# Kernel tuning notes

Measured on AMD Instinct MI355X. Metric: run time of the kernel, lower is better.

The kernel has to match this reference:

```python
import jax, jax.numpy as jnp
import numpy as np

CLIP = 7.0          # cfg.swiglu_clip
AUX_COEF = 0.02     # cfg.router_aux_loss_coef
TOP_K = 4           # cfg.experts_per_token


def setup_inputs() -> dict:
    key = jax.random.key(0)
    ks = jax.random.split(key, 4)
    H, E, FF = 1024, 16, 1024
    B, T = 2, 1024
    std = 0.02
    return {
        "x": jax.random.normal(ks[0], (B, T, H), jnp.float32),
        "W_in": jax.random.normal(ks[1], (E, H, 2 * FF), jnp.float32) * std,
        "b_in": jnp.zeros((E, 2 * FF), jnp.float32),
        "W_out": jax.random.normal(ks[2], (E, FF, H), jnp.float32) * std,
        "b_out": jnp.zeros((E, H), jnp.float32),
        "router_w": jax.random.normal(ks[3], (E, H), jnp.float32) * std,
        "router_b": jnp.zeros((E,), jnp.float32),
    }


def reference(x, W_in, b_in, W_out, b_out, router_w, router_b):
    B, T, H = x.shape
    E = W_in.shape[0]
    S = B * T
    x_flat = x.reshape(S, H)

    # --- router + top-k gating ---
    logits = x_flat @ router_w.T + router_b                         # [S, E]
    topk_w, topk_i = jax.lax.top_k(logits, TOP_K)                   # [S, K]
    topk_w = jax.nn.softmax(topk_w.astype(jnp.float32), axis=-1).astype(x.dtype)

    # --- aux load-balance loss (faithful to source, incl. argmax-over-indices) ---
    probs = jax.nn.softmax(logits.astype(jnp.float32), axis=-1)     # [S, E]
    importance = probs.mean(axis=0)                                 # [E]
    load = jax.nn.one_hot(jnp.argmax(topk_i, axis=-1), E, dtype=jnp.float32).mean(axis=0)
    aux_loss = AUX_COEF * E * jnp.sum(importance * load)

    # scatter top-k weights to dense [S, E] combine weights
    final_w = jnp.zeros((S, E), x.dtype).at[jnp.arange(S)[:, None], topk_i].add(topk_w)

    # --- dense per-expert SwiGLU FFN (every expert for every token) ---
    h = jnp.einsum('sh,ehd->sed', x_flat, W_in) + b_in              # [S, E, 2*FF]
    up, gate = jnp.split(h, 2, axis=-1)                             # chunk(2, -1)
    up = jnp.clip(up, -CLIP, CLIP)
    gate = jnp.clip(gate, -CLIP, CLIP)
    act = jax.nn.silu(gate) * up                                    # [S, E, FF]
    eo = jnp.einsum('sef,efh->seh', act, W_out) + b_out             # [S, E, H]

    out = jnp.einsum('seh,se->sh', eo, final_w).reshape(B, T, H)
    return out, aux_loss
```

## Files before the change

kernel.cpp:

```cpp
#include <hip/hip_runtime.h>
#include <math.h>

#define S_TOK 2048
#define H_DIM 1024
#define E_NUM 16
#define FF_DIM 1024
#define TOPK 4
#define CLIPV 7.0f
#define AUXC 0.02f
#define BK 32
#define NT (H_DIM / BK)

typedef short bf16x8 __attribute__((ext_vector_type(8)));
typedef float f32x4 __attribute__((ext_vector_type(4)));

__device__ __forceinline__ unsigned short f2bf(float f) {
  unsigned int u = __float_as_uint(f);
  u += 0x7fffu + ((u >> 16) & 1u);
  return (unsigned short)(u >> 16);
}

__device__ __forceinline__ void gload16(const void* g, void* l) {
  __builtin_amdgcn_global_load_lds((const __attribute__((address_space(1))) void*)g,
                                   (__attribute__((address_space(3))) void*)l, 16, 0, 0);
}

__device__ __forceinline__ int imin(int a, int b) { return a < b ? a : b; }

__global__ void logits_kernel(const float* __restrict__ x, const float* __restrict__ rw,
                              const float* __restrict__ rb, float* __restrict__ logits,
                              unsigned short* __restrict__ xb) {
  int tok = blockIdx.x * 4 + (threadIdx.x >> 6);
  int lane = threadIdx.x & 63;
  const float4* xr = (const float4*)(x + (size_t)tok * H_DIM);
  ushort4* xbw = (ushort4*)(xb + (size_t)tok * H_DIM);
  float p[E_NUM];
#pragma unroll
  for (int e = 0; e < E_NUM; ++e) p[e] = 0.f;
#pragma unroll
  for (int it = 0; it < 4; ++it) {
    float4 xv = xr[it * 64 + lane];
    ushort4 o;
    o.x = f2bf(xv.x); o.y = f2bf(xv.y); o.z = f2bf(xv.z); o.w = f2bf(xv.w);
    xbw[it * 64 + lane] = o;
#pragma unroll
    for (int e = 0; e < E_NUM; ++e) {
      float4 wv = ((const float4*)(rw + (size_t)e * H_DIM))[it * 64 + lane];
      p[e] += xv.x * wv.x + xv.y * wv.y + xv.z * wv.z + xv.w * wv.w;
    }
  }
#pragma unroll
  for (int e = 0; e < E_NUM; ++e) {
#pragma unroll
    for (int off = 32; off > 0; off >>= 1) p[e] += __shfl_xor(p[e], off);
  }
  if (lane == 0) {
    float4* lp = (float4*)&logits[tok * E_NUM];
#pragma unroll
    for (int q = 0; q < 4; ++q)
      lp[q] = make_float4(p[q * 4 + 0] + rb[q * 4 + 0], p[q * 4 + 1] + rb[q * 4 + 1],
                          p[q * 4 + 2] + rb[q * 4 + 2], p[q * 4 + 3] + rb[q * 4 + 3]);
  }
}

__global__ __launch_bounds__(256) void topk_kernel(const float* __restrict__ logits,
                                                   int* __restrict__ topk_i, float* __restrict__ topk_w,
                                                   int* __restrict__ counts, float* __restrict__ imp,
                                                   int* __restrict__ pos_cnt) {
  __shared__ float s_imp[E_NUM];
  __shared__ int s_cnt[E_NUM];
  __shared__ int s_pos[TOPK];
  int tid = threadIdx.x;
  if (tid < E_NUM) { s_imp[tid] = 0.f; s_cnt[tid] = 0; }
  if (tid < TOPK) s_pos[tid] = 0;
  __syncthreads();

  int t = blockIdx.x * 256 + tid;
  float lg[E_NUM];
  {
    const float4* lp = (const float4*)&logits[t * E_NUM];
#pragma unroll
    for (int q = 0; q < 4; ++q) {
      float4 v = lp[q];
      lg[q * 4 + 0] = v.x; lg[q * 4 + 1] = v.y; lg[q * 4 + 2] = v.z; lg[q * 4 + 3] = v.w;
    }
  }
  int idx[TOPK]; float val[TOPK];
  float tmp[E_NUM];
#pragma unroll
  for (int e = 0; e < E_NUM; ++e) tmp[e] = lg[e];
#pragma unroll
  for (int k = 0; k < TOPK; ++k) {
    float best = -INFINITY; int bi = 0;
#pragma unroll
    for (int e = 0; e < E_NUM; ++e) if (tmp[e] > best) { best = tmp[e]; bi = e; }
    val[k] = best; idx[k] = bi; tmp[bi] = -INFINITY;
  }
  float ssum = 0.f, wv[TOPK];
#pragma unroll
  for (int k = 0; k < TOPK; ++k) { wv[k] = expf(val[k] - val[0]); ssum += wv[k]; }
#pragma unroll
  for (int k = 0; k < TOPK; ++k) wv[k] /= ssum;
#pragma unroll
  for (int k = 0; k < TOPK; ++k) {
    topk_i[t * TOPK + k] = idx[k];
    topk_w[t * TOPK + k] = wv[k];
  }
  float se = 0.f, pr[E_NUM];
#pragma unroll
  for (int e = 0; e < E_NUM; ++e) { pr[e] = expf(lg[e] - val[0]); se += pr[e]; }
  float inv = 1.f / se;
  int mi = idx[0], pos = 0;
#pragma unroll
  for (int k = 1; k < TOPK; ++k) if (idx[k] > mi) { mi = idx[k]; pos = k; }

  int lane = tid & 63;
#pragma unroll
  for (int e = 0; e < E_NUM; ++e) {
    float v = pr[e] * inv;
    int c = (idx[0] == e) + (idx[1] == e) + (idx[2] == e) + (idx[3] == e);
#pragma unroll
    for (int off = 32; off > 0; off >>= 1) {
      v += __shfl_xor(v, off);
      c += __shfl_xor(c, off);
    }
    if (lane == 0) {
      atomicAdd(&s_imp[e], v);
      atomicAdd(&s_cnt[e], c);
    }
  }
#pragma unroll
  for (int k = 0; k < TOPK; ++k) {
    int pc = (pos == k) ? 1 : 0;
#pragma unroll
    for (int off = 32; off > 0; off >>= 1) pc += __shfl_xor(pc, off);
    if (lane == 0) atomicAdd(&s_pos[k], pc);
  }
  __syncthreads();
  if (tid < E_NUM) {
    atomicAdd(&imp[tid], s_imp[tid]);
    atomicAdd(&counts[tid], s_cnt[tid]);
  }
  if (tid < TOPK) atomicAdd(&pos_cnt[tid], s_pos[tid]);
}

__global__ void scan_kernel(const int* __restrict__ counts, int* __restrict__ offsets) {
  if (threadIdx.x == 0) {
    int off = 0;
    for (int e = 0; e < E_NUM; ++e) { offsets[e] = off; off += counts[e]; }
    offsets[E_NUM] = off;
  }
}

__global__ __launch_bounds__(256) void assign_kernel(
    const int* __restrict__ topk_i, const int* __restrict__ offsets, int* __restrict__ cursor,
    int* __restrict__ tok_list, int* __restrict__ slot_of) {
  __shared__ int s_cnt[E_NUM];
  __shared__ int s_base[E_NUM];
  int tid = threadIdx.x;
  if (tid < E_NUM) s_cnt[tid] = 0;
  __syncthreads();
  int t = blockIdx.x * 256 + tid;
  int e[TOPK], lslot[TOPK];
#pragma unroll
  for (int k = 0; k < TOPK; ++k) {
    e[k] = topk_i[t * TOPK + k];
    lslot[k] = atomicAdd(&s_cnt[e[k]], 1);
  }
  __syncthreads();
  if (tid < E_NUM) s_base[tid] = atomicAdd(&cursor[tid], s_cnt[tid]);
  __syncthreads();
#pragma unroll
  for (int k = 0; k < TOPK; ++k) {
    int slot = offsets[e[k]] + s_base[e[k]] + lslot[k];
    tok_list[slot] = t;
    slot_of[t * TOPK + k] = slot;
  }
}

__global__ void transpose_kernel(const float* __restrict__ in, unsigned short* __restrict__ out,
                                 int R, int C) {
  __shared__ float tile[64][65];
  int e = blockIdx.z;
  in  += (size_t)e * R * C;
  out += (size_t)e * R * C;
  int r0 = blockIdx.y * 64, c0 = blockIdx.x * 64;
  int tx = threadIdx.x & 15, ty = threadIdx.x >> 4;
#pragma unroll
  for (int j = 0; j < 4; ++j) {
    int r = ty + j * 16;
    float4 v = *(const float4*)&in[(size_t)(r0 + r) * C + c0 + tx * 4];
    tile[r][tx * 4 + 0] = v.x; tile[r][tx * 4 + 1] = v.y;
    tile[r][tx * 4 + 2] = v.z; tile[r][tx * 4 + 3] = v.w;
  }
  __syncthreads();
#pragma unroll
  for (int j = 0; j < 4; ++j) {
    int c = ty + j * 16;
    ushort4 o;
    o.x = f2bf(tile[tx * 4 + 0][c]);
    o.y = f2bf(tile[tx * 4 + 1][c]);
    o.z = f2bf(tile[tx * 4 + 2][c]);
    o.w = f2bf(tile[tx * 4 + 3][c]);
    *(ushort4*)&out[(size_t)(c0 + c) * R + r0 + tx * 4] = o;
  }
}

__global__ __launch_bounds__(256, 2) void gemm1_kernel(
    const unsigned short* __restrict__ xb, const unsigned short* __restrict__ winT,
    const float* __restrict__ b_in, const int* __restrict__ offsets,
    const int* __restrict__ tok_list, unsigned short* __restrict__ act) {
  __shared__ unsigned short ldsA[2][128 * BK];
  __shared__ unsigned short ldsB[2][256 * BK];
  const int lin = blockIdx.x;
  const int nid = (lin & 7) * 256 + (lin >> 3);
  const int e  = nid >> 7;
  const int mt = (nid & 127) >> 3;
  const int nt = nid & 7;
  const int base = offsets[e];
  const int cnt = offsets[e + 1] - base;
  if (mt * 128 >= cnt) return;
  const int n0f = nt * 128;
  const int tid = threadIdx.x, w = tid >> 6, lane = tid & 63;

  const int arow = w * 16 + (lane >> 2);
  const int t0 = tok_list[base + imin(mt * 128 + arow, cnt - 1)];
  const int t1 = tok_list[base + imin(mt * 128 + arow + 64, cnt - 1)];
  const unsigned short* gA0 = xb + (size_t)t0 * H_DIM + (lane & 3) * 8;
  const unsigned short* gA1 = xb + (size_t)t1 * H_DIM + (lane & 3) * 8;
  auto brow_f = [&](int r) {
    int f = n0f + ((r >> 5) << 4) + (r & 15);
    return ((r >> 4) & 1) ? (FF_DIM + f) : f;
  };
  const unsigned short* we = winT + (size_t)e * 2 * FF_DIM * H_DIM;
  const unsigned short* gB0 = we + (size_t)brow_f(arow)       * H_DIM + (lane & 3) * 8;
  const unsigned short* gB1 = we + (size_t)brow_f(arow + 64)  * H_DIM + (lane & 3) * 8;
  const unsigned short* gB2 = we + (size_t)brow_f(arow + 128) * H_DIM + (lane & 3) * 8;
  const unsigned short* gB3 = we + (size_t)brow_f(arow + 192) * H_DIM + (lane & 3) * 8;

  f32x4 acc[8][4];
#pragma unroll
  for (int m = 0; m < 8; ++m)
#pragma unroll
    for (int n = 0; n < 4; ++n) acc[m][n] = (f32x4){0.f, 0.f, 0.f, 0.f};

#define STAGE1(buf, k0)                                     \
  do {                                                      \
    gload16(gA0 + (k0), &ldsA[buf][w * 512]);               \
    gload16(gA1 + (k0), &ldsA[buf][w * 512 + 2048]);        \
    gload16(gB0 + (k0), &ldsB[buf][w * 512]);               \
    gload16(gB1 + (k0), &ldsB[buf][w * 512 + 2048]);        \
    gload16(gB2 + (k0), &ldsB[buf][w * 512 + 4096]);        \
    gload16(gB3 + (k0), &ldsB[buf][w * 512 + 6144]);        \
  } while (0)

  STAGE1(0, 0);
  __syncthreads();
  int buf = 0;
  const int ko = (lane >> 4) * 8;
  for (int kt = 0; kt < NT; ++kt) {
    if (kt + 1 < NT) STAGE1(buf ^ 1, (kt + 1) * BK);
    bf16x8 a[8], b[4];
#pragma unroll
    for (int mf = 0; mf < 8; ++mf)
      a[mf] = *(const bf16x8*)&ldsA[buf][(mf * 16 + (lane & 15)) * BK + ko];
#pragma unroll
    for (int nf = 0; nf < 4; ++nf)
      b[nf] = *(const bf16x8*)&ldsB[buf][(w * 64 + nf * 16 + (lane & 15)) * BK + ko];
#pragma unroll
    for (int mf = 0; mf < 8; ++mf)
#pragma unroll
      for (int nf = 0; nf < 4; ++nf)
        acc[mf][nf] = __builtin_amdgcn_mfma_f32_16x16x32_bf16(a[mf], b[nf], acc[mf][nf], 0, 0, 0);
    __syncthreads();
    buf ^= 1;
  }

  const float* bin = b_in + (size_t)e * 2 * FF_DIM;
#pragma unroll
  for (int mf = 0; mf < 8; ++mf) {
    int rbase = mf * 16 + (lane >> 4) * 4;
#pragma unroll
    for (int p = 0; p < 2; ++p) {
      int f = n0f + (w * 2 + p) * 16 + (lane & 15);
      float bu = bin[f], bg = bin[FF_DIM + f];
#pragma unroll
      for (int i = 0; i < 4; ++i) {
        int mrow = mt * 128 + rbase + i;
        if (mrow < cnt) {
          float up = acc[mf][2 * p][i] + bu;
          float gt = acc[mf][2 * p + 1][i] + bg;
          up = fminf(fmaxf(up, -CLIPV), CLIPV);
          gt = fminf(fmaxf(gt, -CLIPV), CLIPV);
          float av = (gt / (1.f + expf(-gt))) * up;
          act[(size_t)(base + mrow) * FF_DIM + f] = f2bf(av);
        }
      }
    }
  }
}

__global__ __launch_bounds__(256, 2) void gemm2_kernel(
    const unsigned short* __restrict__ act, const unsigned short* __restrict__ woutT,
    const float* __restrict__ b_out, const int* __restrict__ offsets,
    float* __restrict__ eo) {
  __shared__ unsigned short ldsA[2][128 * BK];
  __shared__ unsigned short ldsB[2][256 * BK];
  const int lin = blockIdx.x;
  const int nid = (lin & 7) * 128 + (lin >> 3);
  const int e = nid >> 6;
  const int rem = nid & 63;
  const int mt = rem >> 2;
  const int nt = rem & 3;
  const int base = offsets[e];
  const int cnt = offsets[e + 1] - base;
  if (mt * 128 >= cnt) return;
  const int n0 = nt * 256;
  const int tid = threadIdx.x, w = tid >> 6, lane = tid & 63;

  const int arow = w * 16 + (lane >> 2);
  const int m0_ = imin(mt * 128 + arow, cnt - 1);
  const int m1_ = imin(mt * 128 + arow + 64, cnt - 1);
  const int kbase = (lane & 3) * 8;
  const unsigned short* gA0 = act + (size_t)(base + m0_) * FF_DIM + kbase;
  const unsigned short* gA1 = act + (size_t)(base + m1_) * FF_DIM + kbase;
  const unsigned short* we = woutT + (size_t)e * H_DIM * FF_DIM;
  const unsigned short* gB0 = we + (size_t)(n0 + arow)       * FF_DIM + kbase;
  const unsigned short* gB1 = we + (size_t)(n0 + arow + 64)  * FF_DIM + kbase;
  const unsigned short* gB2 = we + (size_t)(n0 + arow + 128) * FF_DIM + kbase;
  const unsigned short* gB3 = we + (size_t)(n0 + arow + 192) * FF_DIM + kbase;

  f32x4 acc[8][4];
#pragma unroll
  for (int m = 0; m < 8; ++m)
#pragma unroll
    for (int n = 0; n < 4; ++n) acc[m][n] = (f32x4){0.f, 0.f, 0.f, 0.f};

#define STAGE2(buf, k0)                                     \
  do {                                                      \
    gload16(gA0 + (k0), &ldsA[buf][w * 512]);               \
    gload16(gA1 + (k0), &ldsA[buf][w * 512 + 2048]);        \
    gload16(gB0 + (k0), &ldsB[buf][w * 512]);               \
    gload16(gB1 + (k0), &ldsB[buf][w * 512 + 2048]);        \
    gload16(gB2 + (k0), &ldsB[buf][w * 512 + 4096]);        \
    gload16(gB3 + (k0), &ldsB[buf][w * 512 + 6144]);        \
  } while (0)

  STAGE2(0, 0);
  __syncthreads();
  int buf = 0;
  const int ko = (lane >> 4) * 8;
  for (int kt = 0; kt < FF_DIM / BK; ++kt) {
    if (kt + 1 < FF_DIM / BK) STAGE2(buf ^ 1, (kt + 1) * BK);
    bf16x8 a[8], b[4];
#pragma unroll
    for (int mf = 0; mf < 8; ++mf)
      a[mf] = *(const bf16x8*)&ldsA[buf][(mf * 16 + (lane & 15)) * BK + ko];
#pragma unroll
    for (int nf = 0; nf < 4; ++nf)
      b[nf] = *(const bf16x8*)&ldsB[buf][(w * 64 + nf * 16 + (lane & 15)) * BK + ko];
#pragma unroll
    for (int mf = 0; mf < 8; ++mf)
#pragma unroll
      for (int nf = 0; nf < 4; ++nf)
        acc[mf][nf] = __builtin_amdgcn_mfma_f32_16x16x32_bf16(a[mf], b[nf], acc[mf][nf], 0, 0, 0);
    __syncthreads();
    buf ^= 1;
  }

  const float* bo = b_out + (size_t)e * H_DIM;
#pragma unroll
  for (int mf = 0; mf < 8; ++mf) {
#pragma unroll
    for (int i = 0; i < 4; ++i) {
      int mrow = mt * 128 + mf * 16 + (lane >> 4) * 4 + i;
      if (mrow < cnt) {
        float* row = eo + (size_t)(base + mrow) * H_DIM;
#pragma unroll
        for (int nf = 0; nf < 4; ++nf) {
          int h = n0 + w * 64 + nf * 16 + (lane & 15);
          row[h] = acc[mf][nf][i] + bo[h];
        }
      }
    }
  }
}

__global__ __launch_bounds__(256) void combine_kernel(
    const float* __restrict__ eo, const float* __restrict__ topk_w,
    const int* __restrict__ slot_of, float* __restrict__ out) {
  int t = blockIdx.x;
  int tid = threadIdx.x;
  float4 r = make_float4(0.f, 0.f, 0.f, 0.f);
#pragma unroll
  for (int k = 0; k < TOPK; ++k) {
    int s = slot_of[t * TOPK + k];
    float wv = topk_w[t * TOPK + k];
    float4 v = ((const float4*)(eo + (size_t)s * H_DIM))[tid];
    r.x = fmaf(wv, v.x, r.x);
    r.y = fmaf(wv, v.y, r.y);
    r.z = fmaf(wv, v.z, r.z);
    r.w = fmaf(wv, v.w, r.w);
  }
  ((float4*)(out + (size_t)t * H_DIM))[tid] = r;
}

__global__ void finalize_kernel(const float* __restrict__ imp, const int* __restrict__ pos_cnt,
                                float* __restrict__ out_aux) {
  if (threadIdx.x == 0) {
    float s = 0.f;
    for (int p = 0; p < TOPK; ++p)
      s += (imp[p] / (float)S_TOK) * ((float)pos_cnt[p] / (float)S_TOK);
    *out_aux = AUXC * (float)E_NUM * s;
  }
}

extern "C" void kernel_launch(void* const* d_in, const int* in_sizes, int n_in,
                              void* d_out, int out_size, void* d_ws, size_t ws_size,
                              hipStream_t stream) {
  const float* x     = (const float*)d_in[0];
  const float* W_in  = (const float*)d_in[1];
  const float* b_in  = (const float*)d_in[2];
  const float* W_out = (const float*)d_in[3];
  const float* b_out = (const float*)d_in[4];
  const float* rw    = (const float*)d_in[5];
  const float* rb    = (const float*)d_in[6];
  float* out = (float*)d_out;

  char* ws = (char*)d_ws;
  size_t off = 0;
  auto alloc = [&](size_t bytes) {
    void* p = ws + off;
    off = (off + bytes + 255) & ~(size_t)255;
    return p;
  };
  unsigned short* xb    = (unsigned short*)alloc((size_t)S_TOK * H_DIM * 2);
  unsigned short* winT  = (unsigned short*)alloc((size_t)E_NUM * 2 * FF_DIM * H_DIM * 2);
  unsigned short* woutT = (unsigned short*)alloc((size_t)E_NUM * H_DIM * FF_DIM * 2);
  unsigned short* act   = (unsigned short*)alloc((size_t)S_TOK * TOPK * FF_DIM * 2);
  float* eo      = (float*)alloc((size_t)S_TOK * TOPK * H_DIM * 4);
  float* logits  = (float*)alloc((size_t)S_TOK * E_NUM * 4);
  int*   topk_i  = (int*)alloc(S_TOK * TOPK * 4);
  float* topk_w  = (float*)alloc(S_TOK * TOPK * 4);
  int*   tok_list= (int*)alloc(S_TOK * TOPK * 4);
  int*   slot_of = (int*)alloc(S_TOK * TOPK * 4);
  int* ctrl = (int*)alloc(64 * 4);
  int* counts = ctrl;
  int* cursor = ctrl + 16;
  int* pos_cnt = ctrl + 32;
  float* imp = (float*)(ctrl + 48);
  int* offsets = (int*)alloc(32 * 4);

  hipMemsetAsync(ctrl, 0, 64 * 4, stream);

  logits_kernel<<<S_TOK / 4, 256, 0, stream>>>(x, rw, rb, logits, xb);
  transpose_kernel<<<dim3(2 * FF_DIM / 64, H_DIM / 64, E_NUM), 256, 0, stream>>>(W_in, winT, H_DIM, 2 * FF_DIM);
  transpose_kernel<<<dim3(H_DIM / 64, FF_DIM / 64, E_NUM), 256, 0, stream>>>(W_out, woutT, FF_DIM, H_DIM);
  topk_kernel<<<S_TOK / 256, 256, 0, stream>>>(logits, topk_i, topk_w, counts, imp, pos_cnt);
  scan_kernel<<<1, 64, 0, stream>>>(counts, offsets);
  assign_kernel<<<S_TOK / 256, 256, 0, stream>>>(topk_i, offsets, cursor, tok_list, slot_of);
  gemm1_kernel<<<2048, 256, 0, stream>>>(xb, winT, b_in, offsets, tok_list, act);
  gemm2_kernel<<<1024, 256, 0, stream>>>(act, woutT, b_out, offsets, eo);
  combine_kernel<<<S_TOK, 256, 0, stream>>>(eo, topk_w, slot_of, out);
  finalize_kernel<<<1, 64, 0, stream>>>(imp, pos_cnt, out + (size_t)S_TOK * H_DIM);
}
```

Measured before the change: 224.3 us.

## Triple-buffer LDS pipeline with explicit vmcnt waits and remap tile order

Both grouped GEMM kernels move from double- to triple-buffered LDS staging. They prefetch two K-tiles ahead and use explicit s_waitcnt vmcnt counts plus raw s_barrier in place of __syncthreads, so global loads overlap more with MFMA work. The block-to-tile mapping also changes so that mt is the fastest-varying index, which groups blocks that share weight columns for L2 reuse. The extra LDS buffer (72KB per block) may cut occupancy below the two blocks per CU requested by the launch bounds. The hand-written vmcnt counts are fragile if the compiler reorders or splits the loads.

```diff
diff --git a/kernel.cpp b/kernel.cpp
--- a/kernel.cpp
+++ b/kernel.cpp
@@ -210,13 +210,13 @@
     const unsigned short* __restrict__ xb, const unsigned short* __restrict__ winT,
     const float* __restrict__ b_in, const int* __restrict__ offsets,
     const int* __restrict__ tok_list, unsigned short* __restrict__ act) {
-  __shared__ unsigned short ldsA[2][128 * BK];
-  __shared__ unsigned short ldsB[2][256 * BK];
+  __shared__ unsigned short ldsA[3][128 * BK];
+  __shared__ unsigned short ldsB[3][256 * BK];
   const int lin = blockIdx.x;
   const int nid = (lin & 7) * 256 + (lin >> 3);
   const int e  = nid >> 7;
-  const int mt = (nid & 127) >> 3;
-  const int nt = nid & 7;
+  const int nt = (nid >> 4) & 7;
+  const int mt = nid & 15;
   const int base = offsets[e];
   const int cnt = offsets[e + 1] - base;
   if (mt * 128 >= cnt) return;
@@ -255,12 +255,21 @@
   } while (0)
 
   STAGE1(0, 0);
-  __syncthreads();
+  STAGE1(1, BK);
   int buf = 0;
-  const int ko = (lane >> 4) * 8;
   for (int kt = 0; kt < NT; ++kt) {
-    if (kt + 1 < NT) STAGE1(buf ^ 1, (kt + 1) * BK);
+    int nb = buf + 2; if (nb >= 3) nb -= 3;
+    if (kt + 2 < NT) {
+      STAGE1(nb, (kt + 2) * BK);
+      asm volatile("s_waitcnt vmcnt(12)" ::: "memory");
+    } else if (kt + 2 == NT) {
+      asm volatile("s_waitcnt vmcnt(6)" ::: "memory");
+    } else {
+      asm volatile("s_waitcnt vmcnt(0)" ::: "memory");
+    }
+    __builtin_amdgcn_s_barrier();
     bf16x8 a[8], b[4];
+    const int ko = (lane >> 4) * 8;
 #pragma unroll
     for (int mf = 0; mf < 8; ++mf)
       a[mf] = *(const bf16x8*)&ldsA[buf][(mf * 16 + (lane & 15)) * BK + ko];
@@ -272,8 +281,8 @@
 #pragma unroll
       for (int nf = 0; nf < 4; ++nf)
         acc[mf][nf] = __builtin_amdgcn_mfma_f32_16x16x32_bf16(a[mf], b[nf], acc[mf][nf], 0, 0, 0);
-    __syncthreads();
-    buf ^= 1;
+    __builtin_amdgcn_s_barrier();
+    buf = (buf == 2) ? 0 : buf + 1;
   }
 
   const float* bin = b_in + (size_t)e * 2 * FF_DIM;
@@ -304,14 +313,13 @@
     const unsigned short* __restrict__ act, const unsigned short* __restrict__ woutT,
     const float* __restrict__ b_out, const int* __restrict__ offsets,
     float* __restrict__ eo) {
-  __shared__ unsigned short ldsA[2][128 * BK];
-  __shared__ unsigned short ldsB[2][256 * BK];
+  __shared__ unsigned short ldsA[3][128 * BK];
+  __shared__ unsigned short ldsB[3][256 * BK];
   const int lin = blockIdx.x;
   const int nid = (lin & 7) * 128 + (lin >> 3);
   const int e = nid >> 6;
-  const int rem = nid & 63;
-  const int mt = rem >> 2;
-  const int nt = rem & 3;
+  const int nt = (nid >> 4) & 3;
+  const int mt = nid & 15;
   const int base = offsets[e];
   const int cnt = offsets[e + 1] - base;
   if (mt * 128 >= cnt) return;
@@ -347,12 +355,21 @@
   } while (0)
 
   STAGE2(0, 0);
-  __syncthreads();
+  STAGE2(1, BK);
   int buf = 0;
-  const int ko = (lane >> 4) * 8;
   for (int kt = 0; kt < FF_DIM / BK; ++kt) {
-    if (kt + 1 < FF_DIM / BK) STAGE2(buf ^ 1, (kt + 1) * BK);
+    int nb = buf + 2; if (nb >= 3) nb -= 3;
+    if (kt + 2 < FF_DIM / BK) {
+      STAGE2(nb, (kt + 2) * BK);
+      asm volatile("s_waitcnt vmcnt(12)" ::: "memory");
+    } else if (kt + 2 == FF_DIM / BK) {
+      asm volatile("s_waitcnt vmcnt(6)" ::: "memory");
+    } else {
+      asm volatile("s_waitcnt vmcnt(0)" ::: "memory");
+    }
+    __builtin_amdgcn_s_barrier();
     bf16x8 a[8], b[4];
+    const int ko = (lane >> 4) * 8;
 #pragma unroll
     for (int mf = 0; mf < 8; ++mf)
       a[mf] = *(const bf16x8*)&ldsA[buf][(mf * 16 + (lane & 15)) * BK + ko];
@@ -364,8 +381,8 @@
 #pragma unroll
       for (int nf = 0; nf < 4; ++nf)
         acc[mf][nf] = __builtin_amdgcn_mfma_f32_16x16x32_bf16(a[mf], b[nf], acc[mf][nf], 0, 0, 0);
-    __syncthreads();
-    buf ^= 1;
+    __builtin_amdgcn_s_barrier();
+    buf = (buf == 2) ? 0 : buf + 1;
   }
 
   const float* bo = b_out + (size_t)e * H_DIM;
```

New measurement: 216.3 us. -3.6%, faster.

## Rework expert GEMMs into 8-wave 256x256 tiles with swizzled LDS pipeline

Applied to the files above, without the earlier changes.

Both grouped expert GEMMs now use 512-thread blocks computing 256x256 output tiles. The K loop is split into 32-wide half-steps across a double-buffered 128KB LDS ring, and direct global-to-LDS loads are interleaved phase by phase with MFMA bursts. Explicit barriers, vmcnt waits and s_setprio control the overlap, and an XOR swizzle on LDS chunks is meant to avoid bank conflicts. The aim is more operand reuse per load and better hiding of memory latency behind MFMA work. In exchange, occupancy drops to one block per CU, and the larger M tile can waste more work when an expert's token count is uneven.

```diff
diff --git a/kernel.cpp b/kernel.cpp
--- a/kernel.cpp
+++ b/kernel.cpp
@@ -8,8 +8,6 @@
 #define TOPK 4
 #define CLIPV 7.0f
 #define AUXC 0.02f
-#define BK 32
-#define NT (H_DIM / BK)
 
 typedef short bf16x8 __attribute__((ext_vector_type(8)));
 typedef float f32x4 __attribute__((ext_vector_type(4)));
@@ -206,90 +204,132 @@
   }
 }
 
-__global__ __launch_bounds__(256, 2) void gemm1_kernel(
+#define A_LDS(buf, ks)  (((buf) * 2 + (ks)) * 16384)
+#define B_LDS(buf, ks)  (65536 + ((buf) * 2 + (ks)) * 16384)
+
+#define PHASE(buf, mh, ks, STAGE, VMC)                                          \
+  do {                                                                          \
+    bf16x8 a_[4];                                                               \
+    _Pragma("unroll") for (int m_ = 0; m_ < 4; ++m_)                            \
+      a_[m_] = *(const bf16x8*)(ldsc + A_LDS(buf, ks) +                         \
+                                (lrow_a + ((mh)*4 + m_) * 16) * 64 + lchunk);   \
+    if ((mh) == 0) {                                                            \
+      _Pragma("unroll") for (int n_ = 0; n_ < 4; ++n_)                          \
+        bq[n_] = *(const bf16x8*)(ldsc + B_LDS(buf, ks) +                       \
+                                  (lrow_b + n_ * 16) * 64 + lchunk);            \
+    }                                                                           \
+    STAGE;                                                                      \
+    __builtin_amdgcn_s_barrier();                                               \
+    asm volatile("s_waitcnt lgkmcnt(0)" ::: "memory");                          \
+    __builtin_amdgcn_sched_barrier(0);                                          \
+    __builtin_amdgcn_s_setprio(1);                                              \
+    _Pragma("unroll") for (int m_ = 0; m_ < 4; ++m_)                            \
+      _Pragma("unroll") for (int n_ = 0; n_ < 4; ++n_)                          \
+        acc[(mh)*4 + m_][n_] = __builtin_amdgcn_mfma_f32_16x16x32_bf16(         \
+            a_[m_], bq[n_], acc[(mh)*4 + m_][n_], 0, 0, 0);                     \
+    __builtin_amdgcn_s_setprio(0);                                              \
+    asm volatile("s_waitcnt vmcnt(" #VMC ")" ::: "memory");                     \
+    __builtin_amdgcn_s_barrier();                                               \
+  } while (0)
+
+#define NOP do {} while (0)
+
+__global__ __launch_bounds__(512, 2) void gemm1_kernel(
     const unsigned short* __restrict__ xb, const unsigned short* __restrict__ winT,
     const float* __restrict__ b_in, const int* __restrict__ offsets,
     const int* __restrict__ tok_list, unsigned short* __restrict__ act) {
-  __shared__ unsigned short ldsA[2][128 * BK];
-  __shared__ unsigned short ldsB[2][256 * BK];
+  __shared__ __align__(16) unsigned short lds[65536];
   const int lin = blockIdx.x;
-  const int nid = (lin & 7) * 256 + (lin >> 3);
-  const int e  = nid >> 7;
-  const int mt = (nid & 127) >> 3;
-  const int nt = nid & 7;
+  const int nid = (lin & 7) * 128 + (lin >> 3);
+  const int e  = nid >> 6;
+  const int nt = (nid >> 3) & 7;
+  const int mt = nid & 7;
   const int base = offsets[e];
   const int cnt = offsets[e + 1] - base;
-  if (mt * 128 >= cnt) return;
+  if (mt * 256 >= cnt) return;
   const int n0f = nt * 128;
-  const int tid = threadIdx.x, w = tid >> 6, lane = tid & 63;
-
-  const int arow = w * 16 + (lane >> 2);
-  const int t0 = tok_list[base + imin(mt * 128 + arow, cnt - 1)];
-  const int t1 = tok_list[base + imin(mt * 128 + arow + 64, cnt - 1)];
-  const unsigned short* gA0 = xb + (size_t)t0 * H_DIM + (lane & 3) * 8;
-  const unsigned short* gA1 = xb + (size_t)t1 * H_DIM + (lane & 3) * 8;
+  const int tid = threadIdx.x, W = tid >> 6, l = tid & 63;
+  const int wr = W >> 2, wc = W & 3;
+
+  const int c_src = (l & 3) ^ ((l >> 3) & 3);
+  const int rd0 = (W * 2 + 0) * 16 + (l >> 2);
+  const int rd1 = (W * 2 + 1) * 16 + (l >> 2);
+  const int tA0 = tok_list[base + imin(mt * 256 + rd0, cnt - 1)];
+  const int tA1 = tok_list[base + imin(mt * 256 + rd1, cnt - 1)];
+  const unsigned short* pA0 = xb + (size_t)tA0 * H_DIM + c_src * 8;
+  const unsigned short* pA1 = xb + (size_t)tA1 * H_DIM + c_src * 8;
   auto brow_f = [&](int r) {
     int f = n0f + ((r >> 5) << 4) + (r & 15);
     return ((r >> 4) & 1) ? (FF_DIM + f) : f;
   };
   const unsigned short* we = winT + (size_t)e * 2 * FF_DIM * H_DIM;
-  const unsigned short* gB0 = we + (size_t)brow_f(arow)       * H_DIM + (lane & 3) * 8;
-  const unsigned short* gB1 = we + (size_t)brow_f(arow + 64)  * H_DIM + (lane & 3) * 8;
-  const unsigned short* gB2 = we + (size_t)brow_f(arow + 128) * H_DIM + (lane & 3) * 8;
-  const unsigned short* gB3 = we + (size_t)brow_f(arow + 192) * H_DIM + (lane & 3) * 8;
+  const unsigned short* pB0 = we + (size_t)brow_f(rd0) * H_DIM + c_src * 8;
+  const unsigned short* pB1 = we + (size_t)brow_f(rd1) * H_DIM + c_src * 8;
+  const int sseg = W * 2048;
+
+#define STA(kt, ks, buf)                                                        \
+  do {                                                                          \
+    gload16(pA0 + (kt) * 64 + (ks) * 32, (char*)lds + A_LDS(buf, ks) + sseg);   \
+    gload16(pA1 + (kt) * 64 + (ks) * 32, (char*)lds + A_LDS(buf, ks) + sseg + 1024); \
+  } while (0)
+#define STB(kt, ks, buf)                                                        \
+  do {                                                                          \
+    gload16(pB0 + (kt) * 64 + (ks) * 32, (char*)lds + B_LDS(buf, ks) + sseg);   \
+    gload16(pB1 + (kt) * 64 + (ks) * 32, (char*)lds + B_LDS(buf, ks) + sseg + 1024); \
+  } while (0)
+
+  const char* ldsc = (const char*)lds;
+  const int lrow_a = wr * 128 + (l & 15);
+  const int lrow_b = wc * 64 + (l & 15);
+  const int lchunk = ((l >> 4) * 16) ^ (((l >> 1) & 3) << 4);
 
   f32x4 acc[8][4];
 #pragma unroll
   for (int m = 0; m < 8; ++m)
 #pragma unroll
     for (int n = 0; n < 4; ++n) acc[m][n] = (f32x4){0.f, 0.f, 0.f, 0.f};
-
-#define STAGE1(buf, k0)                                     \
-  do {                                                      \
-    gload16(gA0 + (k0), &ldsA[buf][w * 512]);               \
-    gload16(gA1 + (k0), &ldsA[buf][w * 512 + 2048]);        \
-    gload16(gB0 + (k0), &ldsB[buf][w * 512]);               \
-    gload16(gB1 + (k0), &ldsB[buf][w * 512 + 2048]);        \
-    gload16(gB2 + (k0), &ldsB[buf][w * 512 + 4096]);        \
-    gload16(gB3 + (k0), &ldsB[buf][w * 512 + 6144]);        \
-  } while (0)
-
-  STAGE1(0, 0);
-  __syncthreads();
-  int buf = 0;
-  const int ko = (lane >> 4) * 8;
-  for (int kt = 0; kt < NT; ++kt) {
-    if (kt + 1 < NT) STAGE1(buf ^ 1, (kt + 1) * BK);
-    bf16x8 a[8], b[4];
-#pragma unroll
-    for (int mf = 0; mf < 8; ++mf)
-      a[mf] = *(const bf16x8*)&ldsA[buf][(mf * 16 + (lane & 15)) * BK + ko];
-#pragma unroll
-    for (int nf = 0; nf < 4; ++nf)
-      b[nf] = *(const bf16x8*)&ldsB[buf][(w * 64 + nf * 16 + (lane & 15)) * BK + ko];
-#pragma unroll
-    for (int mf = 0; mf < 8; ++mf)
-#pragma unroll
-      for (int nf = 0; nf < 4; ++nf)
-        acc[mf][nf] = __builtin_amdgcn_mfma_f32_16x16x32_bf16(a[mf], b[nf], acc[mf][nf], 0, 0, 0);
-    __syncthreads();
-    buf ^= 1;
-  }
+  bf16x8 bq[4];
+
+  STA(0, 0, 0); STB(0, 0, 0); STA(0, 1, 0); STB(0, 1, 0); STA(1, 0, 1); STB(1, 0, 1);
+  asm volatile("s_waitcnt vmcnt(8)" ::: "memory");
+  __builtin_amdgcn_s_barrier();
+
+  for (int i = 0; i < 7; ++i) {
+    const int k0 = 2 * i;
+    PHASE(0, 0, 0, STA(k0 + 1, 1, 1), 8);
+    PHASE(0, 1, 0, STB(k0 + 1, 1, 1), 8);
+    PHASE(0, 0, 1, STA(k0 + 2, 0, 0), 8);
+    PHASE(0, 1, 1, STB(k0 + 2, 0, 0), 8);
+    PHASE(1, 0, 0, STA(k0 + 2, 1, 0), 8);
+    PHASE(1, 1, 0, STB(k0 + 2, 1, 0), 8);
+    PHASE(1, 0, 1, STA(k0 + 3, 0, 1), 8);
+    PHASE(1, 1, 1, STB(k0 + 3, 0, 1), 8);
+  }
+  PHASE(0, 0, 0, STA(15, 1, 1), 8);
+  PHASE(0, 1, 0, STB(15, 1, 1), 8);
+  PHASE(0, 0, 1, NOP, 8);
+  PHASE(0, 1, 1, NOP, 4);
+  PHASE(1, 0, 0, NOP, 4);
+  PHASE(1, 1, 0, NOP, 0);
+  PHASE(1, 0, 1, NOP, 0);
+  PHASE(1, 1, 1, NOP, 0);
+#undef STA
+#undef STB
 
   const float* bin = b_in + (size_t)e * 2 * FF_DIM;
 #pragma unroll
-  for (int mf = 0; mf < 8; ++mf) {
-    int rbase = mf * 16 + (lane >> 4) * 4;
+  for (int m = 0; m < 8; ++m) {
+    int mrow0 = mt * 256 + wr * 128 + m * 16 + (l >> 4) * 4;
 #pragma unroll
     for (int p = 0; p < 2; ++p) {
-      int f = n0f + (w * 2 + p) * 16 + (lane & 15);
+      int f = n0f + (wc * 2 + p) * 16 + (l & 15);
       float bu = bin[f], bg = bin[FF_DIM + f];
 #pragma unroll
-      for (int i = 0; i < 4; ++i) {
-        int mrow = mt * 128 + rbase + i;
+      for (int i2 = 0; i2 < 4; ++i2) {
+        int mrow = mrow0 + i2;
         if (mrow < cnt) {
-          float up = acc[mf][2 * p][i] + bu;
-          float gt = acc[mf][2 * p + 1][i] + bg;
+          float up = acc[m][2 * p][i2] + bu;
+          float gt = acc[m][2 * p + 1][i2] + bg;
           up = fminf(fmaxf(up, -CLIPV), CLIPV);
           gt = fminf(fmaxf(gt, -CLIPV), CLIPV);
           float av = (gt / (1.f + expf(-gt))) * up;
@@ -300,86 +340,97 @@
   }
 }
 
-__global__ __launch_bounds__(256, 2) void gemm2_kernel(
+__global__ __launch_bounds__(512, 2) void gemm2_kernel(
     const unsigned short* __restrict__ act, const unsigned short* __restrict__ woutT,
     const float* __restrict__ b_out, const int* __restrict__ offsets,
     float* __restrict__ eo) {
-  __shared__ unsigned short ldsA[2][128 * BK];
-  __shared__ unsigned short ldsB[2][256 * BK];
+  __shared__ __align__(16) unsigned short lds[65536];
   const int lin = blockIdx.x;
-  const int nid = (lin & 7) * 128 + (lin >> 3);
-  const int e = nid >> 6;
-  const int rem = nid & 63;
-  const int mt = rem >> 2;
-  const int nt = rem & 3;
+  const int nid = (lin & 7) * 64 + (lin >> 3);
+  const int e  = nid >> 5;
+  const int nt = (nid >> 3) & 3;
+  const int mt = nid & 7;
   const int base = offsets[e];
   const int cnt = offsets[e + 1] - base;
-  if (mt * 128 >= cnt) return;
+  if (mt * 256 >= cnt) return;
   const int n0 = nt * 256;
-  const int tid = threadIdx.x, w = tid >> 6, lane = tid & 63;
-
-  const int arow = w * 16 + (lane >> 2);
-  const int m0_ = imin(mt * 128 + arow, cnt - 1);
-  const int m1_ = imin(mt * 128 + arow + 64, cnt - 1);
-  const int kbase = (lane & 3) * 8;
-  const unsigned short* gA0 = act + (size_t)(base + m0_) * FF_DIM + kbase;
-  const unsigned short* gA1 = act + (size_t)(base + m1_) * FF_DIM + kbase;
+  const int tid = threadIdx.x, W = tid >> 6, l = tid & 63;
+  const int wr = W >> 2, wc = W & 3;
+
+  const int c_src = (l & 3) ^ ((l >> 3) & 3);
+  const int rd0 = (W * 2 + 0) * 16 + (l >> 2);
+  const int rd1 = (W * 2 + 1) * 16 + (l >> 2);
+  const int r0_ = imin(mt * 256 + rd0, cnt - 1);
+  const int r1_ = imin(mt * 256 + rd1, cnt - 1);
+  const unsigned short* pA0 = act + (size_t)(base + r0_) * FF_DIM + c_src * 8;
+  const unsigned short* pA1 = act + (size_t)(base + r1_) * FF_DIM + c_src * 8;
   const unsigned short* we = woutT + (size_t)e * H_DIM * FF_DIM;
-  const unsigned short* gB0 = we + (size_t)(n0 + arow)       * FF_DIM + kbase;
-  const unsigned short* gB1 = we + (size_t)(n0 + arow + 64)  * FF_DIM + kbase;
-  const unsigned short* gB2 = we + (size_t)(n0 + arow + 128) * FF_DIM + kbase;
-  const unsigned short* gB3 = we + (size_t)(n0 + arow + 192) * FF_DIM + kbase;
+  const unsigned short* pB0 = we + (size_t)(n0 + rd0) * FF_DIM + c_src * 8;
+  const unsigned short* pB1 = we + (size_t)(n0 + rd1) * FF_DIM + c_src * 8;
+  const int sseg = W * 2048;
+
+#define STA(kt, ks, buf)                                                        \
+  do {                                                                          \
+    gload16(pA0 + (kt) * 64 + (ks) * 32, (char*)lds + A_LDS(buf, ks) + sseg);   \
+    gload16(pA1 + (kt) * 64 + (ks) * 32, (char*)lds + A_LDS(buf, ks) + sseg + 1024); \
+  } while (0)
+#define STB(kt, ks, buf)                                                        \
+  do {                                                                          \
+    gload16(pB0 + (kt) * 64 + (ks) * 32, (char*)lds + B_LDS(buf, ks) + sseg);   \
+    gload16(pB1 + (kt) * 64 + (ks) * 32, (char*)lds + B_LDS(buf, ks) + sseg + 1024); \
+  } while (0)
+
+  const char* ldsc = (const char*)lds;
+  const int lrow_a = wr * 128 + (l & 15);
+  const int lrow_b = wc * 64 + (l & 15);
+  const int lchunk = ((l >> 4) * 16) ^ (((l >> 1) & 3) << 4);
 
   f32x4 acc[8][4];
 #pragma unroll
   for (int m = 0; m < 8; ++m)
 #pragma unroll
     for (int n = 0; n < 4; ++n) acc[m][n] = (f32x4){0.f, 0.f, 0.f, 0.f};
-
-#define STAGE2(buf, k0)                                     \
-  do {                                                      \
-    gload16(gA0 + (k0), &ldsA[buf][w * 512]);               \
-    gload16(gA1 + (k0), &ldsA[buf][w * 512 + 2048]);        \
-    gload16(gB0 + (k0), &ldsB[buf][w * 512]);               \
-    gload16(gB1 + (k0), &ldsB[buf][w * 512 + 2048]);        \
-    gload16(gB2 + (k0), &ldsB[buf][w * 512 + 4096]);        \
-    gload16(gB3 + (k0), &ldsB[buf][w * 512 + 6144]);        \
-  } while (0)
-
-  STAGE2(0, 0);
-  __syncthreads();
-  int buf = 0;
-  const int ko = (lane >> 4) * 8;
-  for (int kt = 0; kt < FF_DIM / BK; ++kt) {
-    if (kt + 1 < FF_DIM / BK) STAGE2(buf ^ 1, (kt + 1) * BK);
-    bf16x8 a[8], b[4];
-#pragma unroll
-    for (int mf = 0; mf < 8; ++mf)
-      a[mf] = *(const bf16x8*)&ldsA[buf][(mf * 16 + (lane & 15)) * BK + ko];
-#pragma unroll
-    for (int nf = 0; nf < 4; ++nf)
-      b[nf] = *(const bf16x8*)&ldsB[buf][(w * 64 + nf * 16 + (lane & 15)) * BK + ko];
-#pragma unroll
-    for (int mf = 0; mf < 8; ++mf)
-#pragma unroll
-      for (int nf = 0; nf < 4; ++nf)
-        acc[mf][nf] = __builtin_amdgcn_mfma_f32_16x16x32_bf16(a[mf], b[nf], acc[mf][nf], 0, 0, 0);
-    __syncthreads();
-    buf ^= 1;
-  }
+  bf16x8 bq[4];
+
+  STA(0, 0, 0); STB(0, 0, 0); STA(0, 1, 0); STB(0, 1, 0); STA(1, 0, 1); STB(1, 0, 1);
+  asm volatile("s_waitcnt vmcnt(8)" ::: "memory");
+  __builtin_amdgcn_s_barrier();
+
+  for (int i = 0; i < 7; ++i) {
+    const int k0 = 2 * i;
+    PHASE(0, 0, 0, STA(k0 + 1, 1, 1), 8);
+    PHASE(0, 1, 0, STB(k0 + 1, 1, 1), 8);
+    PHASE(0, 0, 1, STA(k0 + 2, 0, 0), 8);
+    PHASE(0, 1, 1, STB(k0 + 2, 0, 0), 8);
+    PHASE(1, 0, 0, STA(k0 + 2, 1, 0), 8);
+    PHASE(1, 1, 0, STB(k0 + 2, 1, 0), 8);
+    PHASE(1, 0, 1, STA(k0 + 3, 0, 1), 8);
+    PHASE(1, 1, 1, STB(k0 + 3, 0, 1), 8);
+  }
+  PHASE(0, 0, 0, STA(15, 1, 1), 8);
+  PHASE(0, 1, 0, STB(15, 1, 1), 8);
+  PHASE(0, 0, 1, NOP, 8);
+  PHASE(0, 1, 1, NOP, 4);
+  PHASE(1, 0, 0, NOP, 4);
+  PHASE(1, 1, 0, NOP, 0);
+  PHASE(1, 0, 1, NOP, 0);
+  PHASE(1, 1, 1, NOP, 0);
+#undef STA
+#undef STB
 
   const float* bo = b_out + (size_t)e * H_DIM;
 #pragma unroll
-  for (int mf = 0; mf < 8; ++mf) {
-#pragma unroll
-    for (int i = 0; i < 4; ++i) {
-      int mrow = mt * 128 + mf * 16 + (lane >> 4) * 4 + i;
+  for (int m = 0; m < 8; ++m) {
+    int mrow0 = mt * 256 + wr * 128 + m * 16 + (l >> 4) * 4;
+#pragma unroll
+    for (int i2 = 0; i2 < 4; ++i2) {
+      int mrow = mrow0 + i2;
       if (mrow < cnt) {
         float* row = eo + (size_t)(base + mrow) * H_DIM;
 #pragma unroll
-        for (int nf = 0; nf < 4; ++nf) {
-          int h = n0 + w * 64 + nf * 16 + (lane & 15);
-          row[h] = acc[mf][nf][i] + bo[h];
+        for (int n = 0; n < 4; ++n) {
+          int h = n0 + wc * 64 + n * 16 + (l & 15);
+          row[h] = acc[m][n][i2] + bo[h];
         }
       }
     }
@@ -459,8 +510,8 @@
   topk_kernel<<<S_TOK / 256, 256, 0, stream>>>(logits, topk_i, topk_w, counts, imp, pos_cnt);
   scan_kernel<<<1, 64, 0, stream>>>(counts, offsets);
   assign_kernel<<<S_TOK / 256, 256, 0, stream>>>(topk_i, offsets, cursor, tok_list, slot_of);
-  gemm1_kernel<<<2048, 256, 0, stream>>>(xb, winT, b_in, offsets, tok_list, act);
-  gemm2_kernel<<<1024, 256, 0, stream>>>(act, woutT, b_out, offsets, eo);
+  gemm1_kernel<<<1024, 512, 0, stream>>>(xb, winT, b_in, offsets, tok_list, act);
+  gemm2_kernel<<<512, 512, 0, stream>>>(act, woutT, b_out, offsets, eo);
   combine_kernel<<<S_TOK, 256, 0, stream>>>(eo, topk_w, slot_of, out);
   finalize_kernel<<<1, 64, 0, stream>>>(imp, pos_cnt, out + (size_t)S_TOK * H_DIM);
 }
```

Measured after the change: 208.2 us. -7.2%, faster.
